# Kernel tuning notes

Hardware: AMD Instinct MI355X
Metric: run time of the kernel (lower is better)

The kernel has to match this reference:

```python
import jax
jax.config.update("jax_enable_x64", True)  # Sinkhorn runs in f64, matching torch's d.double()
import jax.numpy as jnp
import numpy as np

N, D, K = 32768, 128, 1024
TAU = 0.2
SK_EPS = 0.005
SK_ITERS = 3


def setup_inputs() -> dict:
    key = jax.random.key(0)
    k1, k2 = jax.random.split(key)
    x = jax.random.normal(k1, (N, D), dtype=jnp.float32)
    codebook = jax.random.normal(k2, (K, D), dtype=jnp.float32) * 0.02  # embedding.weight
    return {"x": x, "codebook": codebook}


def _l2norm(v):
    # F.normalize with eps=1e-12
    n = jnp.linalg.norm(v, axis=-1, keepdims=True)
    return v / jnp.maximum(n, 1e-12)


def _center_distance(d):
    d = jnp.where(jnp.isnan(d), jnp.zeros_like(d), d)
    mx, mn = d.max(), d.min()
    middle = (mx + mn) / 2
    amplitude = jnp.maximum(mx - middle + 1e-5, 1e-5)
    return (d - middle) / amplitude


def _sinkhorn(d, epsilon, iters):
    # d: [N, K] in f64; Q: [K, N]
    Q = jnp.exp(-d / epsilon).T
    Kc, B = Q.shape
    Q = Q / jnp.maximum(Q.sum(), 1e-5)

    def body(Q, _):
        Q = Q / Q.sum(axis=1, keepdims=True) / Kc
        Q = Q / Q.sum(axis=0, keepdims=True) / B
        return Q, None

    Q, _ = jax.lax.scan(body, Q, None, length=iters)
    return (Q * B).T  # [N, K]


def reference(x, codebook):
    latent = x.reshape(-1, codebook.shape[-1])  # [N, D]
    cos_sim = _l2norm(latent) @ _l2norm(codebook).T  # [N, K]
    d = (1.0 - cos_sim) / TAU

    # training path with sk_epsilon > 0: center + Sinkhorn (no_grad in torch)
    dc = _center_distance(jax.lax.stop_gradient(d))
    Q = _sinkhorn(dc.astype(jnp.float64), SK_EPS, SK_ITERS)
    indices = jnp.argmax(Q, axis=-1)  # [N]

    x_q = codebook[indices].reshape(x.shape)

    # cross-entropy(cos_sim / tau, indices.detach())
    logits = cos_sim / TAU
    logp = jax.nn.log_softmax(logits, axis=-1)
    loss = -jnp.mean(jnp.take_along_axis(logp, indices[:, None], axis=-1))

    # straight-through estimator
    x_q = x + jax.lax.stop_gradient(x_q - x)
    return x_q, loss, indices
```

## Files before the change

### kernel.cpp

```cpp
#include <hip/hip_runtime.h>
#include <cstddef>

#define NPTS 32768
#define DDIM 128
#define KCB  1024

typedef __attribute__((ext_vector_type(8))) short short8;
typedef __attribute__((ext_vector_type(4))) float f32x4;


__device__ __forceinline__ float hw_exp2(float x) {
#if __has_builtin(__builtin_amdgcn_exp2f)
  return __builtin_amdgcn_exp2f(x);
#else
  return exp2f(x);
#endif
}

__device__ __forceinline__ void atomic_add_f64(double* p, double v) {
  __hip_atomic_fetch_add(p, v, __ATOMIC_RELAXED, __HIP_MEMORY_SCOPE_AGENT);
}

__device__ __forceinline__ unsigned short bf16_rne(float v) {
  unsigned u = __float_as_uint(v);
  unsigned r = u + 0x7FFFu + ((u >> 16) & 1u);
  return (unsigned short)(r >> 16);
}
__device__ __forceinline__ float bf16_tof(unsigned short h) {
  return __uint_as_float((unsigned)h << 16);
}

__device__ __forceinline__ float div_mark(float x, float c, float rc) {
  float q0 = x * rc;
  float r  = fmaf(-c, q0, x);
  return fmaf(r, rc, q0);
}

__device__ __forceinline__ double sweep_E(float cv, float middle, float amp, float rc_amp) {
  float d  = div_mark(1.0f - cv, 0.2f, 1.0f / 0.2f);
  float dc = div_mark(d - middle, amp, rc_amp);
  double xl2 = (double)dc * (-288.53900817779268);
  double kd  = rint(xl2);
  float  fr  = (float)(xl2 - kd);
  float  m   = hw_exp2(fr);
  long long bits = ((long long)(1023 + (int)kd)) << 52;
  return (double)m * __longlong_as_double(bits);
}

__device__ __forceinline__ double score_exponent(float cv, float middle, float amplitude) {
  float d  = (1.0f - cv) / 0.2f;
  float dc = (d - middle) / amplitude;
  return (double)dc * (-(1.0 / 0.005));
}

__device__ __forceinline__ unsigned enc_f32(float f) {
  unsigned u = __float_as_uint(f);
  return (u & 0x80000000u) ? ~u : (u | 0x80000000u);
}
__device__ __forceinline__ float dec_f32(unsigned e) {
  unsigned u = (e & 0x80000000u) ? (e & 0x7FFFFFFFu) : ~e;
  return __uint_as_float(u);
}

__device__ __forceinline__ void calc_scal(const unsigned* maxenc, const unsigned* minenc,
                                          float& middle, float& amplitude, float& rc_amp) {
  float cosmax = dec_f32(*maxenc);
  float cosmin = dec_f32(*minenc);
  float mx_d = (1.0f - cosmin) / 0.2f;
  float mn_d = (1.0f - cosmax) / 0.2f;
  middle = (mx_d + mn_d) / 2.0f;
  amplitude = fmaxf(mx_d - middle + 1e-5f, 1e-5f);
  rc_amp = 1.0f / amplitude;
}


__global__ __launch_bounds__(1024) void vq_init_kernel(double* __restrict__ u123,
                                                       double* __restrict__ loss_part,
                                                       unsigned* __restrict__ maxenc,
                                                       unsigned* __restrict__ minenc) {
  int t = threadIdx.x;
  for (int i = t; i < 3 * KCB; i += 1024) u123[i] = 0.0;
  loss_part[t] = 0.0;
  if (t == 0) {
    *maxenc = 0u;
    *minenc = 0xFFFFFFFFu;
  }
}

__global__ __launch_bounds__(128) void vq_normalize_rows(const float* __restrict__ in,
                                                         float* __restrict__ out) {
  int row = blockIdx.x;
  int t = threadIdx.x;
  float v = in[(size_t)row * DDIM + t];
  float s = v * v;
#pragma unroll
  for (int off = 32; off; off >>= 1) s += __shfl_down(s, off, 64);
  __shared__ float red[2];
  if ((t & 63) == 0) red[t >> 6] = s;
  __syncthreads();
  float norm = sqrtf(red[0] + red[1]);
  out[(size_t)row * DDIM + t] = v / fmaxf(norm, 1e-12f);
}

__global__ __launch_bounds__(128) void vq_normalize_split(const float* __restrict__ in,
                                                          unsigned short* __restrict__ oh,
                                                          unsigned short* __restrict__ ol) {
  int row = blockIdx.x;
  int t = threadIdx.x;
  float v = in[(size_t)row * DDIM + t];
  float s = v * v;
#pragma unroll
  for (int off = 32; off; off >>= 1) s += __shfl_down(s, off, 64);
  __shared__ float red[2];
  if ((t & 63) == 0) red[t >> 6] = s;
  __syncthreads();
  float norm = sqrtf(red[0] + red[1]);
  float xnv = v / fmaxf(norm, 1e-12f);
  unsigned short h = bf16_rne(xnv);
  float fh = bf16_tof(h);
  unsigned short l = bf16_rne(xnv - fh);
  size_t idx = (size_t)row * DDIM + t;
  oh[idx] = h;
  ol[idx] = l;
}


__global__ __launch_bounds__(256, 2) void vq_gemm_mfma(const unsigned short* __restrict__ Ah,
                                                       const unsigned short* __restrict__ Al,
                                                       const unsigned short* __restrict__ Bh,
                                                       const unsigned short* __restrict__ Bl,
                                                       float* __restrict__ Cm,
                                                       unsigned* __restrict__ maxenc,
                                                       unsigned* __restrict__ minenc) {
  __shared__ float redmx[4], redmn[4];
  int tid = threadIdx.x;
  int lane = tid & 63, wv = tid >> 6;
  int wr = wv >> 1, wc = wv & 1;
  int c0 = blockIdx.x * 128;
  int n0 = blockIdx.y * 128;
  int fr = lane & 15;
  int kq = (lane >> 4) * 8;
  f32x4 acc[4][4] = {};

  size_t aoff[4], boff[4];
#pragma unroll
  for (int rt = 0; rt < 4; ++rt)
    aoff[rt] = (size_t)(n0 + wr * 64 + rt * 16 + fr) * DDIM + kq;
#pragma unroll
  for (int ct = 0; ct < 4; ++ct)
    boff[ct] = (size_t)(c0 + wc * 64 + ct * 16 + fr) * DDIM + kq;

#pragma unroll
  for (int ks = 0; ks < 4; ++ks) {
    short8 ah[4], al[4], bh[4], bl[4];
#pragma unroll
    for (int i = 0; i < 4; ++i) {
      ah[i] = *(const short8*)(Ah + aoff[i] + ks * 32);
      al[i] = *(const short8*)(Al + aoff[i] + ks * 32);
      bh[i] = *(const short8*)(Bh + boff[i] + ks * 32);
      bl[i] = *(const short8*)(Bl + boff[i] + ks * 32);
    }
#pragma unroll
    for (int rt = 0; rt < 4; ++rt) {
#pragma unroll
      for (int ct = 0; ct < 4; ++ct) {
        acc[rt][ct] = __builtin_amdgcn_mfma_f32_16x16x32_bf16(ah[rt], bh[ct], acc[rt][ct], 0, 0, 0);
        acc[rt][ct] = __builtin_amdgcn_mfma_f32_16x16x32_bf16(ah[rt], bl[ct], acc[rt][ct], 0, 0, 0);
        acc[rt][ct] = __builtin_amdgcn_mfma_f32_16x16x32_bf16(al[rt], bh[ct], acc[rt][ct], 0, 0, 0);
        acc[rt][ct] = __builtin_amdgcn_mfma_f32_16x16x32_bf16(al[rt], bl[ct], acc[rt][ct], 0, 0, 0);
      }
    }
  }

  float mx = -3.402823466e38f, mn = 3.402823466e38f;
  int orow = (lane >> 4) * 4, ocol = lane & 15;
  int rn0 = n0 + wr * 64, rc0 = c0 + wc * 64;
#pragma unroll
  for (int rt = 0; rt < 4; ++rt) {
#pragma unroll
    for (int ct = 0; ct < 4; ++ct) {
#pragma unroll
      for (int r = 0; r < 4; ++r) {
        float v = acc[rt][ct][r];
        mx = fmaxf(mx, v);
        mn = fminf(mn, v);
        Cm[(size_t)(rn0 + rt * 16 + orow + r) * KCB + (rc0 + ct * 16 + ocol)] = v;
      }
    }
  }
#pragma unroll
  for (int off = 32; off; off >>= 1) {
    mx = fmaxf(mx, __shfl_down(mx, off, 64));
    mn = fminf(mn, __shfl_down(mn, off, 64));
  }
  if (lane == 0) { redmx[wv] = mx; redmn[wv] = mn; }
  __syncthreads();
  if (tid == 0) {
    mx = fmaxf(fmaxf(redmx[0], redmx[1]), fmaxf(redmx[2], redmx[3]));
    mn = fminf(fminf(redmn[0], redmn[1]), fminf(redmn[2], redmn[3]));
    atomicMax(maxenc, enc_f32(mx));
    atomicMin(minenc, enc_f32(mn));
  }
}

#define SROWS 32
#define SRPW  8

__global__ __launch_bounds__(256) void vq_sweep(const float* __restrict__ Cm,
                                                const unsigned* __restrict__ maxenc,
                                                const unsigned* __restrict__ minenc,
                                                const double* __restrict__ Rvec,
                                                const double* __restrict__ alpha_p,
                                                double* __restrict__ u_out) {
  int t = threadIdx.x;
  int lane = t & 63, wv = t >> 6;
  int n0 = blockIdx.x * SROWS + wv * SRPW;
  float middle, amp, rc;
  calc_scal(maxenc, minenc, middle, amp, rc);
  bool hasR = (Rvec != nullptr);
  double Rreg[16];
  double ainv = 0.0;
  if (hasR) {
#pragma unroll
    for (int c = 0; c < 4; ++c)
#pragma unroll
      for (int e = 0; e < 4; ++e) Rreg[c * 4 + e] = Rvec[c * 256 + lane * 4 + e];
    ainv = alpha_p[0] * 32768.0;
  }
  double up[16] = {};
  float4 cva[4], cvb[4];
  {
    const float4* row0 = (const float4*)(Cm + (size_t)n0 * KCB);
#pragma unroll
    for (int c = 0; c < 4; ++c) cva[c] = row0[c * 64 + lane];
  }
#pragma unroll 1
  for (int r = 0; r < SRPW; ++r) {
    int rn = (r < SRPW - 1) ? r + 1 : r;
    const float4* rown = (const float4*)(Cm + (size_t)(n0 + rn) * KCB);
#pragma unroll
    for (int c = 0; c < 4; ++c) cvb[c] = rown[c * 64 + lane];
    double e[16];
#pragma unroll
    for (int c = 0; c < 4; ++c) {
      e[c * 4 + 0] = sweep_E(cva[c].x, middle, amp, rc);
      e[c * 4 + 1] = sweep_E(cva[c].y, middle, amp, rc);
      e[c * 4 + 2] = sweep_E(cva[c].z, middle, amp, rc);
      e[c * 4 + 3] = sweep_E(cva[c].w, middle, amp, rc);
    }
    if (hasR) {
      double s = 0.0;
#pragma unroll
      for (int i = 0; i < 16; ++i) s += e[i] * Rreg[i];
#pragma unroll
      for (int off = 1; off < 64; off <<= 1) s += __shfl_xor(s, off, 64);
      double C = 1.0 / (ainv * s);
#pragma unroll
      for (int i = 0; i < 16; ++i) up[i] += e[i] * C;
    } else {
#pragma unroll
      for (int i = 0; i < 16; ++i) up[i] += e[i];
    }
#pragma unroll
    for (int c = 0; c < 4; ++c) cva[c] = cvb[c];
  }
  __shared__ double su[4][KCB];
#pragma unroll
  for (int c = 0; c < 4; ++c)
#pragma unroll
    for (int e = 0; e < 4; ++e) su[wv][c * 256 + lane * 4 + e] = up[c * 4 + e];
  __syncthreads();
#pragma unroll
  for (int j = 0; j < 4; ++j) {
    int k = (t + ((blockIdx.x + j) & 3) * 256) & (KCB - 1);
    double v = su[0][k] + su[1][k] + su[2][k] + su[3][k];
    atomic_add_f64(&u_out[k], v);
  }
}

__global__ __launch_bounds__(1024) void vq_finalize_u(const double* __restrict__ u,
                                                      double* __restrict__ alpha_p,
                                                      double* __restrict__ R,
                                                      double* __restrict__ lnR,
                                                      int mode) {
  int k = threadIdx.x;
  double uk = u[k];
  __shared__ double red[16];
  __shared__ double s_alpha;
  if (mode == 0) {
    double s = uk;
#pragma unroll
    for (int off = 32; off; off >>= 1) s += __shfl_down(s, off, 64);
    if ((k & 63) == 0) red[k >> 6] = s;
    __syncthreads();
    if (k == 0) {
      double s0 = 0.0;
      for (int w = 0; w < 16; ++w) s0 += red[w];
      double a = 1.0 / fmax(s0, 1e-5);
      s_alpha = a;
      alpha_p[0] = a;
    }
    __syncthreads();
  }
  double alpha = (mode == 0) ? s_alpha : alpha_p[0];
  double r = 1.0 / (alpha * 1024.0 * uk);
  R[k] = r;
  if (mode == 2) lnR[k] = log(r);
}

#define FRPW 4
#define MARGIN 0.08f
#define LOG2E 1.44269504088896340736f

__global__ __launch_bounds__(256) void vq_final_pass(const float* __restrict__ Cm,
                                                     const float* __restrict__ x,
                                                     const float* __restrict__ cb,
                                                     const float* __restrict__ xn,
                                                     const float* __restrict__ cn,
                                                     const double* __restrict__ lnR,
                                                     const unsigned* __restrict__ maxenc,
                                                     const unsigned* __restrict__ minenc,
                                                     double* __restrict__ loss_part,
                                                     float* __restrict__ out_xq,
                                                     float* __restrict__ out_idx) {
  int t = threadIdx.x;
  int lane = t & 63, wv = t >> 6;
  int n0 = blockIdx.x * (4 * FRPW) + wv * FRPW;
  float middle, amplitude, rc_amp;
  calc_scal(maxenc, minenc, middle, amplitude, rc_amp);
  float lnRf[16];
  double lnRd[16];
#pragma unroll
  for (int c = 0; c < 4; ++c)
#pragma unroll
    for (int e = 0; e < 4; ++e) {
      double v = lnR[c * 256 + lane * 4 + e];
      lnRd[c * 4 + e] = v;
      lnRf[c * 4 + e] = (float)v;
    }

  double loss_loc = 0.0;
  float4 cva[4], cvb[4];
  {
    const float4* row0 = (const float4*)(Cm + (size_t)n0 * KCB);
#pragma unroll
    for (int c = 0; c < 4; ++c) cva[c] = row0[c * 64 + lane];
  }
#pragma unroll 1
  for (int r = 0; r < FRPW; ++r) {
    int n = n0 + r;
    int rn = (r < FRPW - 1) ? r + 1 : r;
    const float4* rown = (const float4*)(Cm + (size_t)(n0 + rn) * KCB);
#pragma unroll
    for (int c = 0; c < 4; ++c) cvb[c] = rown[c * 64 + lane];

    float lv[16];
    float sv[16];
    float b1 = -3.402823466e38f, b2 = -3.402823466e38f;
    int k1 = 0;
    float lmax = -3.402823466e38f;
#pragma unroll
    for (int c = 0; c < 4; ++c) {
#pragma unroll
      for (int e = 0; e < 4; ++e) {
        float cvv = (e == 0) ? cva[c].x : (e == 1) ? cva[c].y : (e == 2) ? cva[c].z : cva[c].w;
        int k = c * 256 + lane * 4 + e;
        float d  = div_mark(1.0f - cvv, 0.2f, 5.0f);
        float dc = div_mark(d - middle, amplitude, rc_amp);
        float s  = fmaf(dc, -200.0f, lnRf[c * 4 + e]);
        sv[c * 4 + e] = s;
        if (s > b1) { b2 = b1; b1 = s; k1 = k; }
        else if (s > b2) b2 = s;
        float l = div_mark(cvv, 0.2f, 5.0f);
        lv[c * 4 + e] = l;
        lmax = fmaxf(lmax, l);
      }
    }
#pragma unroll
    for (int off = 1; off < 64; off <<= 1) {
      float o1 = __shfl_xor(b1, off, 64);
      int ok = __shfl_xor(k1, off, 64);
      float o2 = __shfl_xor(b2, off, 64);
      float om = __shfl_xor(lmax, off, 64);
      float cand2;
      if (o1 > b1 || (o1 == b1 && ok < k1)) { cand2 = fmaxf(b1, o2); b1 = o1; k1 = ok; }
      else cand2 = fmaxf(o1, o2);
      b2 = fmaxf(b2, cand2);
      lmax = fmaxf(lmax, om);
    }
    int bestk = k1;
    if (b1 - b2 < MARGIN) {
      double pbest = -1.0e308;
      int pk = KCB;
      const float* xr = xn + (size_t)n * DDIM;
      float thr = b1 - MARGIN;
#pragma unroll 1
      for (int i = 0; i < 16; ++i) {
        if (sv[i] >= thr) {
          int k = (i >> 2) * 256 + lane * 4 + (i & 3);
          const float* cr = cn + (size_t)k * DDIM;
          float dot = 0.0f;
          for (int d = 0; d < DDIM; ++d) dot = fmaf(xr[d], cr[d], dot);
          double ps = score_exponent(dot, middle, amplitude) + lnRd[i];
          if (ps > pbest || (ps == pbest && k < pk)) { pbest = ps; pk = k; }
        }
      }
#pragma unroll
      for (int off = 1; off < 64; off <<= 1) {
        double ob = __shfl_xor(pbest, off, 64);
        int ok = __shfl_xor(pk, off, 64);
        if (ob > pbest || (ob == pbest && ok < pk)) { pbest = ob; pk = ok; }
      }
      bestk = pk;
    }
    float se = 0.0f;
    float lb = 0.0f;
#pragma unroll
    for (int c = 0; c < 4; ++c) {
#pragma unroll
      for (int e = 0; e < 4; ++e) {
        int k = c * 256 + lane * 4 + e;
        se += hw_exp2((lv[c * 4 + e] - lmax) * LOG2E);
        if (k == bestk) lb = lv[c * 4 + e];
      }
    }
#pragma unroll
    for (int off = 1; off < 64; off <<= 1) {
      se += __shfl_xor(se, off, 64);
      lb += __shfl_xor(lb, off, 64);
    }
    loss_loc += (double)(-(lb - lmax - logf(se)));
    if (lane == 0) out_idx[n] = (float)bestk;
    float2 xv = *(const float2*)&x[(size_t)n * DDIM + lane * 2];
    float2 cbv = *(const float2*)&cb[(size_t)bestk * DDIM + lane * 2];
    float2 o;
    o.x = xv.x + (cbv.x - xv.x);
    o.y = xv.y + (cbv.y - xv.y);
    *(float2*)&out_xq[(size_t)n * DDIM + lane * 2] = o;
#pragma unroll
    for (int c = 0; c < 4; ++c) cva[c] = cvb[c];
  }
  if (lane == 0) atomic_add_f64(&loss_part[(blockIdx.x * 4 + wv) & (KCB - 1)], loss_loc);
}

__global__ __launch_bounds__(1024) void vq_loss_div(const double* __restrict__ lp,
                                                    float* __restrict__ out_loss) {
  int t = threadIdx.x;
  double s = lp[t];
#pragma unroll
  for (int off = 32; off; off >>= 1) s += __shfl_down(s, off, 64);
  __shared__ double red[16];
  if ((t & 63) == 0) red[t >> 6] = s;
  __syncthreads();
  if (t == 0) {
    double tot = 0.0;
    for (int w = 0; w < 16; ++w) tot += red[w];
    out_loss[0] = (float)(tot / 32768.0);
  }
}


extern "C" void kernel_launch(void* const* d_in, const int* in_sizes, int n_in,
                              void* d_out, int out_size, void* d_ws, size_t ws_size,
                              hipStream_t stream) {
  const float* x  = (const float*)d_in[0];
  const float* cb = (const float*)d_in[1];
  float* out = (float*)d_out;
  float* out_xq   = out;
  float* out_loss = out + (size_t)NPTS * DDIM;
  float* out_idx  = out + (size_t)NPTS * DDIM + 1;

  char* w = (char*)d_ws;
  unsigned short* xh = (unsigned short*)w;
  unsigned short* xl = xh + (size_t)NPTS * DDIM;
  unsigned short* ch = xl + (size_t)NPTS * DDIM;
  unsigned short* cl = ch + (size_t)KCB * DDIM;
  float* xn = (float*)w;
  float* cn = xn + (size_t)NPTS * DDIM;
  float* cosm = (float*)(w + (size_t)16896 * 1024);
  double* u1  = (double*)(cosm + (size_t)NPTS * KCB);
  double* u2  = u1 + KCB;
  double* u3  = u2 + KCB;
  double* R   = u3 + KCB;
  double* lnR = R + KCB;
  double* loss_part = lnR + KCB;
  double* alpha_p   = loss_part + KCB;
  unsigned* maxenc = (unsigned*)(alpha_p + 1);
  unsigned* minenc = maxenc + 1;

  vq_init_kernel<<<1, 1024, 0, stream>>>(u1, loss_part, maxenc, minenc);

  vq_normalize_split<<<NPTS, 128, 0, stream>>>(x, xh, xl);
  vq_normalize_split<<<KCB, 128, 0, stream>>>(cb, ch, cl);
  vq_gemm_mfma<<<dim3(KCB / 128, NPTS / 128), 256, 0, stream>>>(xh, xl, ch, cl, cosm,
                                                                maxenc, minenc);

  vq_normalize_rows<<<NPTS, 128, 0, stream>>>(x, xn);
  vq_normalize_rows<<<KCB, 128, 0, stream>>>(cb, cn);

  vq_sweep<<<NPTS / SROWS, 256, 0, stream>>>(cosm, maxenc, minenc, nullptr, alpha_p, u1);
  vq_finalize_u<<<1, 1024, 0, stream>>>(u1, alpha_p, R, lnR, 0);
  vq_sweep<<<NPTS / SROWS, 256, 0, stream>>>(cosm, maxenc, minenc, R, alpha_p, u2);
  vq_finalize_u<<<1, 1024, 0, stream>>>(u2, alpha_p, R, lnR, 1);
  vq_sweep<<<NPTS / SROWS, 256, 0, stream>>>(cosm, maxenc, minenc, R, alpha_p, u3);
  vq_finalize_u<<<1, 1024, 0, stream>>>(u3, alpha_p, R, lnR, 2);

  vq_final_pass<<<NPTS / (4 * FRPW), 256, 0, stream>>>(cosm, x, cb, xn, cn, lnR,
                                                       maxenc, minenc,
                                                       loss_part, out_xq, out_idx);
  vq_loss_div<<<1, 1024, 0, stream>>>(loss_part, out_loss);
}
```

Measured before the change: 355.1 us.

## Stage GEMM operands through triple-buffered swizzled LDS with async global loads

The split-bf16 MFMA GEMM now copies A/B tiles into a three-deep LDS ring buffer using global_load_lds async copies with an XOR swizzle, overlapping the next stage's loads with the current MFMAs. The block tile shrinks to 128x64, the grid is reordered so consecutive blocks share a codebook tile, and occupancy is raised to 4 blocks per CU. Previously each wave loaded its fragments straight from global memory with no reuse across waves. This adds barrier synchronisation and hand-placed vmcnt waits, which could be fragile if the compiler reorders loads.

```diff
diff --git a/kernel.cpp b/kernel.cpp
--- a/kernel.cpp
+++ b/kernel.cpp
@@ -72,6 +72,21 @@
   amplitude = fmaxf(mx_d - middle + 1e-5f, 1e-5f);
   rc_amp = 1.0f / amplitude;
 }
+
+#if __has_builtin(__builtin_amdgcn_global_load_lds)
+#define HAVE_ASYNC_LDS 1
+typedef __attribute__((address_space(3))) unsigned int lds_u32_t;
+typedef const __attribute__((address_space(1))) unsigned int glb_u32_t;
+__device__ __forceinline__ void async_ld16(const void* g, void* l) {
+  __builtin_amdgcn_global_load_lds((glb_u32_t*)g, (lds_u32_t*)l, 16, 0, 0);
+}
+#else
+#define HAVE_ASYNC_LDS 0
+#endif
+
+#define WAITVM3() asm volatile("s_waitcnt vmcnt(3)" ::: "memory")
+#define WAITVM0() asm volatile("s_waitcnt vmcnt(0)" ::: "memory")
+#define CFENCE()  asm volatile("" ::: "memory")
 
 
 __global__ __launch_bounds__(1024) void vq_init_kernel(double* __restrict__ u123,
@@ -125,60 +140,97 @@
 }
 
 
-__global__ __launch_bounds__(256, 2) void vq_gemm_mfma(const unsigned short* __restrict__ Ah,
+__global__ __launch_bounds__(256, 4) void vq_gemm_mfma(const unsigned short* __restrict__ Ah,
                                                        const unsigned short* __restrict__ Al,
                                                        const unsigned short* __restrict__ Bh,
                                                        const unsigned short* __restrict__ Bl,
                                                        float* __restrict__ Cm,
                                                        unsigned* __restrict__ maxenc,
                                                        unsigned* __restrict__ minenc) {
+  __shared__ unsigned short ldsb[3][6144];
   __shared__ float redmx[4], redmn[4];
   int tid = threadIdx.x;
   int lane = tid & 63, wv = tid >> 6;
   int wr = wv >> 1, wc = wv & 1;
-  int c0 = blockIdx.x * 128;
-  int n0 = blockIdx.y * 128;
+  int n0 = blockIdx.x * 128;
+  int c0 = blockIdx.y * 64;
   int fr = lane & 15;
-  int kq = (lane >> 4) * 8;
-  f32x4 acc[4][4] = {};
-
-  size_t aoff[4], boff[4];
-#pragma unroll
-  for (int rt = 0; rt < 4; ++rt)
-    aoff[rt] = (size_t)(n0 + wr * 64 + rt * 16 + fr) * DDIM + kq;
-#pragma unroll
-  for (int ct = 0; ct < 4; ++ct)
-    boff[ct] = (size_t)(c0 + wc * 64 + ct * 16 + fr) * DDIM + kq;
-
-#pragma unroll
-  for (int ks = 0; ks < 4; ++ks) {
-    short8 ah[4], al[4], bh[4], bl[4];
-#pragma unroll
-    for (int i = 0; i < 4; ++i) {
-      ah[i] = *(const short8*)(Ah + aoff[i] + ks * 32);
-      al[i] = *(const short8*)(Al + aoff[i] + ks * 32);
-      bh[i] = *(const short8*)(Bh + boff[i] + ks * 32);
-      bl[i] = *(const short8*)(Bl + boff[i] + ks * 32);
-    }
+  int sub = lane >> 4;
+  f32x4 acc[4][2] = {};
+
+  auto stage = [&](int ks, int half, int b) {
+    const unsigned short* Ap = half ? Al : Ah;
+    const unsigned short* Bp = half ? Bl : Bh;
+    int kc = ks * 32;
+#pragma unroll
+    for (int l = 0; l < 3; ++l) {
+      int idx = tid + l * 256;
+      int isB = idx >> 9;
+      int row = (idx & 511) >> 2;
+      int ssub = idx & 3;
+      int gsub = ssub ^ ((row >> 1) & 3);
+      const unsigned short* gp = isB ? Bp + (size_t)(c0 + row) * DDIM + kc + gsub * 8
+                                     : Ap + (size_t)(n0 + row) * DDIM + kc + gsub * 8;
+#if HAVE_ASYNC_LDS
+      int wslot = l * 256 + wv * 64;
+      async_ld16(gp, &ldsb[b][wslot * 8]);
+#else
+      *(short8*)&ldsb[b][idx * 8] = *(const short8*)gp;
+#endif
+    }
+  };
+
+  stage(0, 0, 0);
+  stage(0, 1, 1);
+
+  short8 ah[4], al[4], bh[2], bl[2];
+#pragma unroll
+  for (int s = 0; s < 8; ++s) {
+    const int half = s & 1;
+    const int b = s % 3;
+    if (s < 7) WAITVM3(); else WAITVM0();
+    __builtin_amdgcn_s_barrier();
+    CFENCE();
 #pragma unroll
     for (int rt = 0; rt < 4; ++rt) {
-#pragma unroll
-      for (int ct = 0; ct < 4; ++ct) {
-        acc[rt][ct] = __builtin_amdgcn_mfma_f32_16x16x32_bf16(ah[rt], bh[ct], acc[rt][ct], 0, 0, 0);
-        acc[rt][ct] = __builtin_amdgcn_mfma_f32_16x16x32_bf16(ah[rt], bl[ct], acc[rt][ct], 0, 0, 0);
-        acc[rt][ct] = __builtin_amdgcn_mfma_f32_16x16x32_bf16(al[rt], bh[ct], acc[rt][ct], 0, 0, 0);
-        acc[rt][ct] = __builtin_amdgcn_mfma_f32_16x16x32_bf16(al[rt], bl[ct], acc[rt][ct], 0, 0, 0);
-      }
+      int row = wr * 64 + rt * 16 + fr;
+      int slot = row * 4 + (sub ^ ((row >> 1) & 3));
+      if (half == 0) ah[rt] = *(const short8*)&ldsb[b][slot * 8];
+      else           al[rt] = *(const short8*)&ldsb[b][slot * 8];
+    }
+#pragma unroll
+    for (int ct = 0; ct < 2; ++ct) {
+      int row = wc * 32 + ct * 16 + fr;
+      int slot = 512 + row * 4 + (sub ^ ((row >> 1) & 3));
+      if (half == 0) bh[ct] = *(const short8*)&ldsb[b][slot * 8];
+      else           bl[ct] = *(const short8*)&ldsb[b][slot * 8];
+    }
+    if (s < 6) stage((s + 2) >> 1, half, (s + 2) % 3);
+    if (half == 0) {
+#pragma unroll
+      for (int rt = 0; rt < 4; ++rt)
+#pragma unroll
+        for (int ct = 0; ct < 2; ++ct)
+          acc[rt][ct] = __builtin_amdgcn_mfma_f32_16x16x32_bf16(ah[rt], bh[ct], acc[rt][ct], 0, 0, 0);
+    } else {
+#pragma unroll
+      for (int rt = 0; rt < 4; ++rt)
+#pragma unroll
+        for (int ct = 0; ct < 2; ++ct) {
+          acc[rt][ct] = __builtin_amdgcn_mfma_f32_16x16x32_bf16(ah[rt], bl[ct], acc[rt][ct], 0, 0, 0);
+          acc[rt][ct] = __builtin_amdgcn_mfma_f32_16x16x32_bf16(al[rt], bh[ct], acc[rt][ct], 0, 0, 0);
+          acc[rt][ct] = __builtin_amdgcn_mfma_f32_16x16x32_bf16(al[rt], bl[ct], acc[rt][ct], 0, 0, 0);
+        }
     }
   }
 
   float mx = -3.402823466e38f, mn = 3.402823466e38f;
   int orow = (lane >> 4) * 4, ocol = lane & 15;
-  int rn0 = n0 + wr * 64, rc0 = c0 + wc * 64;
+  int rn0 = n0 + wr * 64, rc0 = c0 + wc * 32;
 #pragma unroll
   for (int rt = 0; rt < 4; ++rt) {
 #pragma unroll
-    for (int ct = 0; ct < 4; ++ct) {
+    for (int ct = 0; ct < 2; ++ct) {
 #pragma unroll
       for (int r = 0; r < 4; ++r) {
         float v = acc[rt][ct][r];
@@ -492,8 +544,8 @@
 
   vq_normalize_split<<<NPTS, 128, 0, stream>>>(x, xh, xl);
   vq_normalize_split<<<KCB, 128, 0, stream>>>(cb, ch, cl);
-  vq_gemm_mfma<<<dim3(KCB / 128, NPTS / 128), 256, 0, stream>>>(xh, xl, ch, cl, cosm,
-                                                                maxenc, minenc);
+  vq_gemm_mfma<<<dim3(NPTS / 128, KCB / 64), 256, 0, stream>>>(xh, xl, ch, cl, cosm,
+                                                               maxenc, minenc);
 
   vq_normalize_rows<<<NPTS, 128, 0, stream>>>(x, xn);
   vq_normalize_rows<<<KCB, 128, 0, stream>>>(cb, cn);
```

Measured after the change: 370.5 us. 1.04x slower.

## Restructure split-bf16 GEMM with LDS-staged 256x256 tiles and async pipelining

Applied to the files above, without the earlier changes.

The cosine-similarity GEMM now computes 256x256 output tiles with 512 threads and stages A and B operand slices into swizzled LDS buffers. It uses a 4-deep async global-to-LDS pipeline with vmcnt waits and barriers, and raises MFMA priority with setprio. Before, each wave loaded its fragments straight from global memory with no sharing. The intent is more operand reuse across waves and overlap of loads with MFMA work, paid for with more LDS, more barriers and higher register pressure from 32 accumulators per wave.

```diff
diff --git a/kernel.cpp b/kernel.cpp
--- a/kernel.cpp
+++ b/kernel.cpp
@@ -72,6 +72,23 @@
   amplitude = fmaxf(mx_d - middle + 1e-5f, 1e-5f);
   rc_amp = 1.0f / amplitude;
 }
+
+#if __has_builtin(__builtin_amdgcn_global_load_lds)
+#define HAVE_ASYNC_LDS 1
+typedef __attribute__((address_space(3))) unsigned int lds_u32_t;
+typedef const __attribute__((address_space(1))) unsigned int glb_u32_t;
+__device__ __forceinline__ void async_ld16(const void* g, void* l) {
+  __builtin_amdgcn_global_load_lds((glb_u32_t*)g, (lds_u32_t*)l, 16, 0, 0);
+}
+#else
+#define HAVE_ASYNC_LDS 0
+#endif
+
+#define WAITVM8() asm volatile("s_waitcnt vmcnt(8)" ::: "memory")
+#define WAITVM4() asm volatile("s_waitcnt vmcnt(4)" ::: "memory")
+#define WAITVM0() asm volatile("s_waitcnt vmcnt(0)" ::: "memory")
+#define CFENCE()  asm volatile("" ::: "memory")
+#define SBAR()    do { CFENCE(); __builtin_amdgcn_s_barrier(); CFENCE(); } while (0)
 
 
 __global__ __launch_bounds__(1024) void vq_init_kernel(double* __restrict__ u123,
@@ -125,58 +142,101 @@
 }
 
 
-__global__ __launch_bounds__(256, 2) void vq_gemm_mfma(const unsigned short* __restrict__ Ah,
+__global__ __launch_bounds__(512, 2) void vq_gemm_mfma(const unsigned short* __restrict__ Ah,
                                                        const unsigned short* __restrict__ Al,
                                                        const unsigned short* __restrict__ Bh,
                                                        const unsigned short* __restrict__ Bl,
                                                        float* __restrict__ Cm,
                                                        unsigned* __restrict__ maxenc,
                                                        unsigned* __restrict__ minenc) {
-  __shared__ float redmx[4], redmn[4];
+  __shared__ unsigned short Ab[4][8192];
+  __shared__ unsigned short Bb[4][8192];
+  __shared__ float redmx[8], redmn[8];
   int tid = threadIdx.x;
   int lane = tid & 63, wv = tid >> 6;
-  int wr = wv >> 1, wc = wv & 1;
-  int c0 = blockIdx.x * 128;
-  int n0 = blockIdx.y * 128;
+  int wm = wv >> 2, wn = wv & 3;
+  int n0 = blockIdx.x * 256;
+  int c0 = blockIdx.y * 256;
   int fr = lane & 15;
-  int kq = (lane >> 4) * 8;
-  f32x4 acc[4][4] = {};
-
-  size_t aoff[4], boff[4];
-#pragma unroll
-  for (int rt = 0; rt < 4; ++rt)
-    aoff[rt] = (size_t)(n0 + wr * 64 + rt * 16 + fr) * DDIM + kq;
-#pragma unroll
-  for (int ct = 0; ct < 4; ++ct)
-    boff[ct] = (size_t)(c0 + wc * 64 + ct * 16 + fr) * DDIM + kq;
-
-#pragma unroll
-  for (int ks = 0; ks < 4; ++ks) {
-    short8 ah[4], al[4], bh[4], bl[4];
-#pragma unroll
-    for (int i = 0; i < 4; ++i) {
-      ah[i] = *(const short8*)(Ah + aoff[i] + ks * 32);
-      al[i] = *(const short8*)(Al + aoff[i] + ks * 32);
-      bh[i] = *(const short8*)(Bh + boff[i] + ks * 32);
-      bl[i] = *(const short8*)(Bl + boff[i] + ks * 32);
-    }
-#pragma unroll
-    for (int rt = 0; rt < 4; ++rt) {
-#pragma unroll
-      for (int ct = 0; ct < 4; ++ct) {
-        acc[rt][ct] = __builtin_amdgcn_mfma_f32_16x16x32_bf16(ah[rt], bh[ct], acc[rt][ct], 0, 0, 0);
-        acc[rt][ct] = __builtin_amdgcn_mfma_f32_16x16x32_bf16(ah[rt], bl[ct], acc[rt][ct], 0, 0, 0);
-        acc[rt][ct] = __builtin_amdgcn_mfma_f32_16x16x32_bf16(al[rt], bh[ct], acc[rt][ct], 0, 0, 0);
-        acc[rt][ct] = __builtin_amdgcn_mfma_f32_16x16x32_bf16(al[rt], bl[ct], acc[rt][ct], 0, 0, 0);
-      }
-    }
+  int swz8 = (((lane >> 4) ^ ((lane >> 1) & 3))) * 8;
+  int arow = (wm * 128 + fr) * 32 + swz8;
+  int brow = (wn * 64 + fr) * 32 + swz8;
+  int srcj8 = (((tid & 3) ^ ((tid >> 3) & 3))) * 8;
+  int r0 = tid >> 2;
+  f32x4 acc[8][4] = {};
+
+  auto stageA = [&](int t) {
+    const unsigned short* p = ((t & 3) < 2) ? Ah : Al;
+    const unsigned short* g = p + (size_t)(n0 + r0) * DDIM + (t >> 2) * 32 + srcj8;
+    unsigned short* lb = &Ab[t & 3][wv * 512];
+#if HAVE_ASYNC_LDS
+    async_ld16(g, lb);
+    async_ld16(g + (size_t)128 * DDIM, lb + 4096);
+#else
+    *(short8*)(&Ab[t & 3][tid * 8])        = *(const short8*)g;
+    *(short8*)(&Ab[t & 3][4096 + tid * 8]) = *(const short8*)(g + (size_t)128 * DDIM);
+#endif
+  };
+  auto stageB = [&](int t) {
+    const unsigned short* p = (t & 1) ? Bl : Bh;
+    const unsigned short* g = p + (size_t)(c0 + r0) * DDIM + (t >> 2) * 32 + srcj8;
+    unsigned short* lb = &Bb[t & 3][wv * 512];
+#if HAVE_ASYNC_LDS
+    async_ld16(g, lb);
+    async_ld16(g + (size_t)128 * DDIM, lb + 4096);
+#else
+    *(short8*)(&Bb[t & 3][tid * 8])        = *(const short8*)g;
+    *(short8*)(&Bb[t & 3][4096 + tid * 8]) = *(const short8*)(g + (size_t)128 * DDIM);
+#endif
+  };
+
+  stageA(0); stageB(0);
+  stageA(1); stageB(1);
+  stageA(2); stageB(2);
+  WAITVM8();
+  SBAR();
+
+  short8 af[4], bf[4];
+#pragma unroll
+  for (int t = 0; t < 16; ++t) {
+    const unsigned short* ab = &Ab[t & 3][0];
+    const unsigned short* bb = &Bb[t & 3][0];
+#pragma unroll
+    for (int ct = 0; ct < 4; ++ct) bf[ct] = *(const short8*)(bb + brow + ct * 512);
+#pragma unroll
+    for (int rt = 0; rt < 4; ++rt) af[rt] = *(const short8*)(ab + arow + rt * 512);
+    if (t <= 12) stageA(t + 3);
+    SBAR();
+    __builtin_amdgcn_s_setprio(1);
+#pragma unroll
+    for (int rt = 0; rt < 4; ++rt)
+#pragma unroll
+      for (int ct = 0; ct < 4; ++ct)
+        acc[rt][ct] = __builtin_amdgcn_mfma_f32_16x16x32_bf16(af[rt], bf[ct], acc[rt][ct], 0, 0, 0);
+    __builtin_amdgcn_s_setprio(0);
+    SBAR();
+#pragma unroll
+    for (int rt = 0; rt < 4; ++rt) af[rt] = *(const short8*)(ab + arow + (rt + 4) * 512);
+    if (t <= 12) stageB(t + 3);
+    SBAR();
+    __builtin_amdgcn_s_setprio(1);
+#pragma unroll
+    for (int rt = 0; rt < 4; ++rt)
+#pragma unroll
+      for (int ct = 0; ct < 4; ++ct)
+        acc[rt + 4][ct] = __builtin_amdgcn_mfma_f32_16x16x32_bf16(af[rt], bf[ct], acc[rt + 4][ct], 0, 0, 0);
+    __builtin_amdgcn_s_setprio(0);
+    if (t <= 12) WAITVM8();
+    else if (t == 13) WAITVM4();
+    else if (t == 14) WAITVM0();
+    SBAR();
   }
 
   float mx = -3.402823466e38f, mn = 3.402823466e38f;
   int orow = (lane >> 4) * 4, ocol = lane & 15;
-  int rn0 = n0 + wr * 64, rc0 = c0 + wc * 64;
-#pragma unroll
-  for (int rt = 0; rt < 4; ++rt) {
+  int rn0 = n0 + wm * 128, rc0 = c0 + wn * 64;
+#pragma unroll
+  for (int rt = 0; rt < 8; ++rt) {
 #pragma unroll
     for (int ct = 0; ct < 4; ++ct) {
 #pragma unroll
@@ -196,8 +256,13 @@
   if (lane == 0) { redmx[wv] = mx; redmn[wv] = mn; }
   __syncthreads();
   if (tid == 0) {
-    mx = fmaxf(fmaxf(redmx[0], redmx[1]), fmaxf(redmx[2], redmx[3]));
-    mn = fminf(fminf(redmn[0], redmn[1]), fminf(redmn[2], redmn[3]));
+#pragma unroll
+    for (int w = 1; w < 8; ++w) {
+      mx = fmaxf(mx, redmx[w]);
+      mn = fminf(mn, redmn[w]);
+    }
+    mx = fmaxf(mx, redmx[0]);
+    mn = fminf(mn, redmn[0]);
     atomicMax(maxenc, enc_f32(mx));
     atomicMin(minenc, enc_f32(mn));
   }
@@ -492,7 +557,7 @@
 
   vq_normalize_split<<<NPTS, 128, 0, stream>>>(x, xh, xl);
   vq_normalize_split<<<KCB, 128, 0, stream>>>(cb, ch, cl);
-  vq_gemm_mfma<<<dim3(KCB / 128, NPTS / 128), 256, 0, stream>>>(xh, xl, ch, cl, cosm,
+  vq_gemm_mfma<<<dim3(NPTS / 256, KCB / 256), 512, 0, stream>>>(xh, xl, ch, cl, cosm,
                                                                 maxenc, minenc);
 
   vq_normalize_rows<<<NPTS, 128, 0, stream>>>(x, xn);
```

Measured after the change: 319.9 us. 1.11x faster.
